# Kernel tuning notes

Measured on AMD Instinct MI355X. Metric: run time of the kernel, lower is better.

## Reference

```python
import jax, jax.numpy as jnp
import numpy as np


def setup_inputs() -> dict:
    key = jax.random.key(0)
    k1, k2, k3 = jax.random.split(key, 3)
    b, c, h, w = 4, 64, 64, 64
    content = jax.random.normal(k1, (b, c, h, w), dtype=jnp.float32)
    content_s = jax.random.normal(k2, (b, c, h, w), dtype=jnp.float32)
    style = jax.random.normal(k3, (b, c, h, w), dtype=jnp.float32)
    return {"content": content, "content_s": content_s, "style": style}


def reference(content, content_s, style):
    b, c, h, w = content.shape
    hw = h * w
    Fc = content.reshape(b, c, hw)      # [b, c, HW]
    Fs = content_s.reshape(b, c, hw)    # [b, c, HW]
    Fst = style.reshape(b, c, hw)       # [b, c, HW]
    # S[b, q, k] = sum_c Fc[b, c, q] * Fs[b, c, k]  (Fc transposed as in torch)
    S = jnp.einsum('bcq,bck->bqk', Fc, Fs)
    S = jax.nn.softmax(S, axis=-1)
    # O = style @ S^T : O[b, c, q] = sum_k Fst[b, c, k] * S[b, q, k]
    O = jnp.einsum('bck,bqk->bcq', Fst, S).reshape(b, c, h, w)
    return jnp.concatenate((content, O), axis=1)
```

## Files before the change

### kernel.cpp

```cpp
#include <hip/hip_runtime.h>
#include <math.h>


#define Bb 4
#define Cc 64
#define HWs 4096
#define RLOG2E 1.44269504088896340736f
#define DEFER_THR 6.0f

typedef _Float16 half8 __attribute__((ext_vector_type(8)));
typedef _Float16 half4 __attribute__((ext_vector_type(4)));
typedef float floatx4 __attribute__((ext_vector_type(4)));
typedef unsigned uint2v __attribute__((ext_vector_type(2)));

__global__ __launch_bounds__(256) void prep_k(const float* __restrict__ content,
                                              const float* __restrict__ Fs,
                                              const float* __restrict__ Fst,
                                              float* __restrict__ out,
                                              _Float16* __restrict__ Kt,
                                              _Float16* __restrict__ Vt) {
    const int bid = blockIdx.x;
    const int t = threadIdx.x;
    if (bid < 1024) {
        int i4 = bid * 256 + t;
        const float4* c4 = (const float4*)content;
        const float4* v4 = (const float4*)Fst;
        float4* o4 = (float4*)out;
        int b = i4 >> 16, rem = i4 & 65535;
        o4[(size_t)b * 131072 + rem] = c4[i4];
        float4 v = v4[i4];
        half4 h;
        h[0] = (_Float16)v.x; h[1] = (_Float16)v.y;
        h[2] = (_Float16)v.z; h[3] = (_Float16)v.w;
        *(half4*)(Vt + (size_t)i4 * 4) = h;
    } else {
        __shared__ _Float16 T[16][72];
        int e = bid - 1024;
        int b = e >> 8;
        int hw0 = (e & 255) * 16;
        const float* sb = Fs + (size_t)b * Cc * HWs;
        {
            int c = t >> 2, x4 = (t & 3) * 4;
            float4 v = *(const float4*)(sb + (size_t)c * HWs + hw0 + x4);
            T[x4 + 0][c] = (_Float16)v.x;
            T[x4 + 1][c] = (_Float16)v.y;
            T[x4 + 2][c] = (_Float16)v.z;
            T[x4 + 3][c] = (_Float16)v.w;
        }
        __syncthreads();
        if (t < 128) {
            int row = t >> 3, g = t & 7;
            _Float16* db = Kt + (size_t)b * HWs * Cc;
            *(half8*)(db + (size_t)(hw0 + row) * Cc + g * 8) = *(half8*)&T[row][g * 8];
        }
    }
}

template <int NS>
__global__ __launch_bounds__(256, 4) void attn_k(const float* __restrict__ Fc,
                                                 const _Float16* __restrict__ Kt,
                                                 const _Float16* __restrict__ Vt,
                                                 _Float16* __restrict__ Opart,
                                                 float2* __restrict__ ml) {
    constexpr int TPS = 64 / NS;
    const int tid  = threadIdx.x;
    const int w    = tid >> 6;
    const int lane = tid & 63;
    const int quad = lane >> 4;
    const int l15  = lane & 15;
    const int qg = blockIdx.x & 31;
    const int b  = (blockIdx.x >> 5) & 3;
    const int s  = blockIdx.x >> 7;
    const int k0base = s * TPS * 64;
    const int qA = qg * 128 + w * 32 + l15;
    const int qB = qA + 16;

    __shared__ _Float16 Kl[2][64 * 64];
    __shared__ _Float16 Vl[2][64 * 64];

    const float*    Fcb = Fc + (size_t)b * Cc * HWs;
    const _Float16* Kb  = Kt + (size_t)b * HWs * Cc;
    const _Float16* Vb  = Vt + (size_t)b * Cc * HWs;

    const bool isK  = tid < 128;
    const int  sl   = tid & 127;
    const int  srow = sl >> 3;
    const int  sjg  = sl & 7;
    const int  ssw  = (sjg ^ (srow & 7)) * 8;

    half8 qf[2][2];
    #pragma unroll
    for (int j = 0; j < 8; ++j) {
        qf[0][0][j] = (_Float16)(Fcb[(size_t)(quad * 8 + j) * HWs + qA] * RLOG2E);
        qf[0][1][j] = (_Float16)(Fcb[(size_t)(32 + quad * 8 + j) * HWs + qA] * RLOG2E);
        qf[1][0][j] = (_Float16)(Fcb[(size_t)(quad * 8 + j) * HWs + qB] * RLOG2E);
        qf[1][1][j] = (_Float16)(Fcb[(size_t)(32 + quad * 8 + j) * HWs + qB] * RLOG2E);
    }

    half8 st[4];
    auto stage_load = [&](int kt) {
        int kk0 = k0base + kt * 64;
        #pragma unroll
        for (int i = 0; i < 4; ++i) {
            int row = srow + 16 * i;
            if (isK) st[i] = *(const half8*)(Kb + (size_t)(kk0 + row) * 64 + sjg * 8);
            else     st[i] = *(const half8*)(Vb + (size_t)row * HWs + kk0 + sjg * 8);
        }
    };
    auto stage_write = [&](int p) {
        #pragma unroll
        for (int i = 0; i < 4; ++i) {
            int row = srow + 16 * i;
            if (isK) *(half8*)&Kl[p][row * 64 + ssw] = st[i];
            else     *(half8*)&Vl[p][row * 64 + ssw] = st[i];
        }
    };

    floatx4 acc[2][4];
    floatx4 accl[2];
    #pragma unroll
    for (int g = 0; g < 2; ++g) {
        accl[g] = (floatx4)(0.0f);
        #pragma unroll
        for (int m = 0; m < 4; ++m) acc[g][m] = (floatx4)(0.0f);
    }
    float m_run[2] = {-INFINITY, -INFINITY};

    half8 vone;
    #pragma unroll
    for (int j = 0; j < 8; ++j) vone[j] = (_Float16)1.0f;

    stage_load(0);
    stage_write(0);
    stage_load(1);
    __syncthreads();

    const int swl = (l15 & 7);
    for (int kt = 0; kt < TPS; ++kt) {
        const int p = kt & 1;
        if (kt + 1 < TPS) stage_write(p ^ 1);
        if (kt + 2 < TPS) stage_load(kt + 2);

        floatx4 sv[2][4];
        #pragma unroll
        for (int m = 0; m < 4; ++m) {
            const half8 ka0 = *(const half8*)&Kl[p][(m * 16 + l15) * 64 + ((quad ^ swl) * 8)];
            const half8 ka1 = *(const half8*)&Kl[p][(m * 16 + l15) * 64 + (((4 + quad) ^ swl) * 8)];
            sv[0][m] = __builtin_amdgcn_mfma_f32_16x16x32_f16(ka0, qf[0][0], (floatx4)(0.0f), 0, 0, 0);
            sv[0][m] = __builtin_amdgcn_mfma_f32_16x16x32_f16(ka1, qf[0][1], sv[0][m], 0, 0, 0);
            sv[1][m] = __builtin_amdgcn_mfma_f32_16x16x32_f16(ka0, qf[1][0], (floatx4)(0.0f), 0, 0, 0);
            sv[1][m] = __builtin_amdgcn_mfma_f32_16x16x32_f16(ka1, qf[1][1], sv[1][m], 0, 0, 0);
        }

        half8 pb[2][2];
        #pragma unroll
        for (int g = 0; g < 2; ++g) {
            float mx = sv[g][0][0];
            #pragma unroll
            for (int m = 0; m < 4; ++m)
                #pragma unroll
                for (int r = 0; r < 4; ++r) mx = fmaxf(mx, sv[g][m][r]);
            {
                unsigned mu = __float_as_uint(mx);
                uint2v t32 = __builtin_amdgcn_permlane32_swap(mu, mu, false, false);
                mx = fmaxf(__uint_as_float(t32[0]), __uint_as_float(t32[1]));
                mu = __float_as_uint(mx);
                uint2v t16 = __builtin_amdgcn_permlane16_swap(mu, mu, false, false);
                mx = fmaxf(__uint_as_float(t16[0]), __uint_as_float(t16[1]));
            }
            if (!__all(mx - m_run[g] <= DEFER_THR)) {
                float m_new = fmaxf(m_run[g], mx);
                float alpha = exp2f(m_run[g] - m_new);
                m_run[g] = m_new;
                #pragma unroll
                for (int m = 0; m < 4; ++m) acc[g][m] *= alpha;
                accl[g] *= alpha;
            }
            const float mb = m_run[g];
            unsigned Ap[4], Bp[4];
            #pragma unroll
            for (int m = 0; m < 4; ++m) {
                float e0 = exp2f(sv[g][m][0] - mb);
                float e1 = exp2f(sv[g][m][1] - mb);
                float e2 = exp2f(sv[g][m][2] - mb);
                float e3 = exp2f(sv[g][m][3] - mb);
                Ap[m] = __builtin_bit_cast(unsigned, __builtin_amdgcn_cvt_pkrtz(e0, e1));
                Bp[m] = __builtin_bit_cast(unsigned, __builtin_amdgcn_cvt_pkrtz(e2, e3));
            }
            unsigned pw[2][4];
            { uint2v a = __builtin_amdgcn_permlane32_swap(Ap[0], Ap[1], false, false);
              uint2v u = __builtin_amdgcn_permlane16_swap(a[0], a[1], false, false);
              pw[0][0] = u[0]; pw[0][2] = u[1]; }
            { uint2v a = __builtin_amdgcn_permlane32_swap(Bp[0], Bp[1], false, false);
              uint2v u = __builtin_amdgcn_permlane16_swap(a[0], a[1], false, false);
              pw[0][1] = u[0]; pw[0][3] = u[1]; }
            { uint2v a = __builtin_amdgcn_permlane32_swap(Ap[2], Ap[3], false, false);
              uint2v u = __builtin_amdgcn_permlane16_swap(a[0], a[1], false, false);
              pw[1][0] = u[0]; pw[1][2] = u[1]; }
            { uint2v a = __builtin_amdgcn_permlane32_swap(Bp[2], Bp[3], false, false);
              uint2v u = __builtin_amdgcn_permlane16_swap(a[0], a[1], false, false);
              pw[1][1] = u[0]; pw[1][3] = u[1]; }
            #pragma unroll
            for (int ks = 0; ks < 2; ++ks) {
                union { unsigned u4[4]; half8 h; } z;
                z.u4[0] = pw[ks][0]; z.u4[1] = pw[ks][1];
                z.u4[2] = pw[ks][2]; z.u4[3] = pw[ks][3];
                pb[g][ks] = z.h;
            }
        }

        #pragma unroll
        for (int m = 0; m < 4; ++m) {
            const half8 va0 = *(const half8*)&Vl[p][(m * 16 + l15) * 64 + ((quad ^ swl) * 8)];
            const half8 va1 = *(const half8*)&Vl[p][(m * 16 + l15) * 64 + (((4 + quad) ^ swl) * 8)];
            acc[0][m] = __builtin_amdgcn_mfma_f32_16x16x32_f16(va0, pb[0][0], acc[0][m], 0, 0, 0);
            acc[0][m] = __builtin_amdgcn_mfma_f32_16x16x32_f16(va1, pb[0][1], acc[0][m], 0, 0, 0);
            acc[1][m] = __builtin_amdgcn_mfma_f32_16x16x32_f16(va0, pb[1][0], acc[1][m], 0, 0, 0);
            acc[1][m] = __builtin_amdgcn_mfma_f32_16x16x32_f16(va1, pb[1][1], acc[1][m], 0, 0, 0);
        }
        accl[0] = __builtin_amdgcn_mfma_f32_16x16x32_f16(vone, pb[0][0], accl[0], 0, 0, 0);
        accl[0] = __builtin_amdgcn_mfma_f32_16x16x32_f16(vone, pb[0][1], accl[0], 0, 0, 0);
        accl[1] = __builtin_amdgcn_mfma_f32_16x16x32_f16(vone, pb[1][0], accl[1], 0, 0, 0);
        accl[1] = __builtin_amdgcn_mfma_f32_16x16x32_f16(vone, pb[1][1], accl[1], 0, 0, 0);

        __syncthreads();
    }

    _Float16* op = Opart + ((size_t)(s * Bb + b) * Cc) * HWs;
    #pragma unroll
    for (int g = 0; g < 2; ++g) {
        int q = (g == 0) ? qA : qB;
        #pragma unroll
        for (int m = 0; m < 4; ++m)
            #pragma unroll
            for (int r = 0; r < 4; ++r) {
                int c = m * 16 + quad * 4 + r;
                op[(size_t)c * HWs + q] = (_Float16)acc[g][m][r];
            }
        if (quad == 0)
            ml[((size_t)b * HWs + q) * NS + s] = make_float2(m_run[g], accl[g][0]);
    }
}

template <int NS>
__global__ __launch_bounds__(256) void combine_k(const _Float16* __restrict__ Opart,
                                                 const float2* __restrict__ ml,
                                                 float* __restrict__ out) {
    int idx = blockIdx.x * 256 + threadIdx.x;
    int q = idx & 4095;
    int c = (idx >> 12) & 63;
    int b = idx >> 18;
    const float2* mlp = ml + ((size_t)b * HWs + q) * NS;
    float2 mls[NS];
    #pragma unroll
    for (int s = 0; s < NS; ++s) mls[s] = mlp[s];
    float M = -INFINITY;
    #pragma unroll
    for (int s = 0; s < NS; ++s) M = fmaxf(M, mls[s].x);
    float l = 0.0f, o = 0.0f;
    #pragma unroll
    for (int s = 0; s < NS; ++s) {
        float wgt = exp2f(mls[s].x - M);
        l += wgt * mls[s].y;
        o += wgt * (float)Opart[(((size_t)s * Bb + b) * Cc + c) * HWs + q];
    }
    out[((size_t)b * 2 * Cc + Cc + c) * HWs + q] = o / l;
}

extern "C" void kernel_launch(void* const* d_in, const int* in_sizes, int n_in,
                              void* d_out, int out_size, void* d_ws, size_t ws_size,
                              hipStream_t stream) {
    const float* content   = (const float*)d_in[0];
    const float* content_s = (const float*)d_in[1];
    const float* style     = (const float*)d_in[2];
    float* out = (float*)d_out;

    _Float16* Kt = (_Float16*)d_ws;
    _Float16* Vt = Kt + (size_t)Bb * HWs * Cc;
    _Float16* Opart = Vt + (size_t)Bb * Cc * HWs;

    const size_t base = (size_t)2 * Bb * HWs * Cc * sizeof(_Float16);
    const size_t need8 = base + (size_t)8 * Bb * Cc * HWs * sizeof(_Float16)
                              + (size_t)Bb * HWs * 8 * sizeof(float2);
    const int ns = (ws_size >= need8) ? 8 : 4;
    float2* ml = (float2*)(Opart + (size_t)ns * Bb * Cc * HWs);

    prep_k<<<dim3(2048), dim3(256), 0, stream>>>(content, content_s, style, out, Kt, Vt);
    if (ns == 8) {
        attn_k<8><<<dim3(8 * Bb * 32), dim3(256), 0, stream>>>(content, Kt, Vt, Opart, ml);
        combine_k<8><<<dim3(4096), dim3(256), 0, stream>>>(Opart, ml, out);
    } else {
        attn_k<4><<<dim3(4 * Bb * 32), dim3(256), 0, stream>>>(content, Kt, Vt, Opart, ml);
        combine_k<4><<<dim3(4096), dim3(256), 0, stream>>>(Opart, ml, out);
    }
}
```

Measured before the change: 112.7 us.

## Stage K/V tiles via direct global-to-LDS loads, sum softmax rows in VALU

Replaces the register-staged K/V tile copy (global load into registers, then LDS write) with the global_load_lds builtin, so all four waves asynchronously fill the next LDS buffer one tile ahead. The row-sum is now accumulated with scalar float adds plus a final shuffle reduction instead of extra MFMA against a ones vector, and s_setprio raises wave priority around the MFMA sections. This is meant to free registers and issue slots and to cut MFMA work, at the cost of a shallower prefetch. The row sum now uses the fp32 exponentials rather than the fp16-rounded values used in the PV product.

```diff
diff --git a/kernel.cpp b/kernel.cpp
--- a/kernel.cpp
+++ b/kernel.cpp
@@ -82,11 +82,26 @@
     const _Float16* Kb  = Kt + (size_t)b * HWs * Cc;
     const _Float16* Vb  = Vt + (size_t)b * Cc * HWs;
 
-    const bool isK  = tid < 128;
-    const int  sl   = tid & 127;
-    const int  srow = sl >> 3;
-    const int  sjg  = sl & 7;
-    const int  ssw  = (sjg ^ (srow & 7)) * 8;
+    const int lrow = lane >> 3;
+    const int lj   = lane & 7;
+    const int lsw8 = (lj ^ lrow) * 8;
+    const int r0   = w * 16;
+
+    auto stage = [&](int kt, int p) {
+        const int kk0 = k0base + kt * 64;
+        #pragma unroll
+        for (int c = 0; c < 2; ++c) {
+            const int r = r0 + c * 8 + lrow;
+            __builtin_amdgcn_global_load_lds(
+                (const __attribute__((address_space(1))) void*)(Kb + (size_t)(kk0 + r) * 64 + lsw8),
+                (__attribute__((address_space(3))) void*)&Kl[p][(r0 + c * 8) * 64],
+                16, 0, 0);
+            __builtin_amdgcn_global_load_lds(
+                (const __attribute__((address_space(1))) void*)(Vb + (size_t)r * HWs + kk0 + lsw8),
+                (__attribute__((address_space(3))) void*)&Vl[p][(r0 + c * 8) * 64],
+                16, 0, 0);
+        }
+    };
 
     half8 qf[2][2];
     #pragma unroll
@@ -97,51 +112,24 @@
         qf[1][1][j] = (_Float16)(Fcb[(size_t)(32 + quad * 8 + j) * HWs + qB] * RLOG2E);
     }
 
-    half8 st[4];
-    auto stage_load = [&](int kt) {
-        int kk0 = k0base + kt * 64;
-        #pragma unroll
-        for (int i = 0; i < 4; ++i) {
-            int row = srow + 16 * i;
-            if (isK) st[i] = *(const half8*)(Kb + (size_t)(kk0 + row) * 64 + sjg * 8);
-            else     st[i] = *(const half8*)(Vb + (size_t)row * HWs + kk0 + sjg * 8);
-        }
-    };
-    auto stage_write = [&](int p) {
-        #pragma unroll
-        for (int i = 0; i < 4; ++i) {
-            int row = srow + 16 * i;
-            if (isK) *(half8*)&Kl[p][row * 64 + ssw] = st[i];
-            else     *(half8*)&Vl[p][row * 64 + ssw] = st[i];
-        }
-    };
-
     floatx4 acc[2][4];
-    floatx4 accl[2];
-    #pragma unroll
-    for (int g = 0; g < 2; ++g) {
-        accl[g] = (floatx4)(0.0f);
+    #pragma unroll
+    for (int g = 0; g < 2; ++g)
         #pragma unroll
         for (int m = 0; m < 4; ++m) acc[g][m] = (floatx4)(0.0f);
-    }
     float m_run[2] = {-INFINITY, -INFINITY};
-
-    half8 vone;
-    #pragma unroll
-    for (int j = 0; j < 8; ++j) vone[j] = (_Float16)1.0f;
-
-    stage_load(0);
-    stage_write(0);
-    stage_load(1);
+    float lsum[2] = {0.0f, 0.0f};
+
+    stage(0, 0);
     __syncthreads();
 
     const int swl = (l15 & 7);
     for (int kt = 0; kt < TPS; ++kt) {
         const int p = kt & 1;
-        if (kt + 1 < TPS) stage_write(p ^ 1);
-        if (kt + 2 < TPS) stage_load(kt + 2);
+        if (kt + 1 < TPS) stage(kt + 1, p ^ 1);
 
         floatx4 sv[2][4];
+        __builtin_amdgcn_s_setprio(1);
         #pragma unroll
         for (int m = 0; m < 4; ++m) {
             const half8 ka0 = *(const half8*)&Kl[p][(m * 16 + l15) * 64 + ((quad ^ swl) * 8)];
@@ -151,6 +139,7 @@
             sv[1][m] = __builtin_amdgcn_mfma_f32_16x16x32_f16(ka0, qf[1][0], (floatx4)(0.0f), 0, 0, 0);
             sv[1][m] = __builtin_amdgcn_mfma_f32_16x16x32_f16(ka1, qf[1][1], sv[1][m], 0, 0, 0);
         }
+        __builtin_amdgcn_s_setprio(0);
 
         half8 pb[2][2];
         #pragma unroll
@@ -174,7 +163,7 @@
                 m_run[g] = m_new;
                 #pragma unroll
                 for (int m = 0; m < 4; ++m) acc[g][m] *= alpha;
-                accl[g] *= alpha;
+                lsum[g] *= alpha;
             }
             const float mb = m_run[g];
             unsigned Ap[4], Bp[4];
@@ -184,6 +173,7 @@
                 float e1 = exp2f(sv[g][m][1] - mb);
                 float e2 = exp2f(sv[g][m][2] - mb);
                 float e3 = exp2f(sv[g][m][3] - mb);
+                lsum[g] += (e0 + e1) + (e2 + e3);
                 Ap[m] = __builtin_bit_cast(unsigned, __builtin_amdgcn_cvt_pkrtz(e0, e1));
                 Bp[m] = __builtin_bit_cast(unsigned, __builtin_amdgcn_cvt_pkrtz(e2, e3));
             }
@@ -209,6 +199,7 @@
             }
         }
 
+        __builtin_amdgcn_s_setprio(1);
         #pragma unroll
         for (int m = 0; m < 4; ++m) {
             const half8 va0 = *(const half8*)&Vl[p][(m * 16 + l15) * 64 + ((quad ^ swl) * 8)];
@@ -218,10 +209,7 @@
             acc[1][m] = __builtin_amdgcn_mfma_f32_16x16x32_f16(va0, pb[1][0], acc[1][m], 0, 0, 0);
             acc[1][m] = __builtin_amdgcn_mfma_f32_16x16x32_f16(va1, pb[1][1], acc[1][m], 0, 0, 0);
         }
-        accl[0] = __builtin_amdgcn_mfma_f32_16x16x32_f16(vone, pb[0][0], accl[0], 0, 0, 0);
-        accl[0] = __builtin_amdgcn_mfma_f32_16x16x32_f16(vone, pb[0][1], accl[0], 0, 0, 0);
-        accl[1] = __builtin_amdgcn_mfma_f32_16x16x32_f16(vone, pb[1][0], accl[1], 0, 0, 0);
-        accl[1] = __builtin_amdgcn_mfma_f32_16x16x32_f16(vone, pb[1][1], accl[1], 0, 0, 0);
+        __builtin_amdgcn_s_setprio(0);
 
         __syncthreads();
     }
@@ -229,6 +217,8 @@
     _Float16* op = Opart + ((size_t)(s * Bb + b) * Cc) * HWs;
     #pragma unroll
     for (int g = 0; g < 2; ++g) {
+        lsum[g] += __shfl_xor(lsum[g], 16);
+        lsum[g] += __shfl_xor(lsum[g], 32);
         int q = (g == 0) ? qA : qB;
         #pragma unroll
         for (int m = 0; m < 4; ++m)
@@ -238,7 +228,7 @@
                 op[(size_t)c * HWs + q] = (_Float16)acc[g][m][r];
             }
         if (quad == 0)
-            ml[((size_t)b * HWs + q) * NS + s] = make_float2(m_run[g], accl[g][0]);
+            ml[((size_t)b * HWs + q) * NS + s] = make_float2(m_run[g], lsum[g]);
     }
 }
 
```

Result: no change. 111.2 us (-1.3%).

## Fold running max into MFMA init, fix four splits, use native exp2

Applied to the files above, without the earlier changes.

The attention kernel now starts the QK MFMA accumulators at -m_run, so scores come out already shifted and the per-element subtraction before exp goes away. The threshold check now runs on the per-lane max before the cross-lane reduction, which skips the permlane work when no rescale is needed. The split count is fixed at 4 rather than chosen at runtime (8 when workspace allows), launch bounds drop to 2 waves, V fragments are loaded before the softmax, and exp2f is replaced by the hardware exp2 intrinsic. The cost is a smaller grid of 512 blocks with twice the serial work per block, plus slightly lower exp precision; m_run starting at 0 instead of -inf changes the max-tracking semantics.

```diff
diff --git a/kernel.cpp b/kernel.cpp
--- a/kernel.cpp
+++ b/kernel.cpp
@@ -5,6 +5,8 @@
 #define Bb 4
 #define Cc 64
 #define HWs 4096
+#define SPLITS 4
+#define TILES_PER_SPLIT 16
 #define RLOG2E 1.44269504088896340736f
 #define DEFER_THR 6.0f
 
@@ -12,6 +14,13 @@
 typedef _Float16 half4 __attribute__((ext_vector_type(4)));
 typedef float floatx4 __attribute__((ext_vector_type(4)));
 typedef unsigned uint2v __attribute__((ext_vector_type(2)));
+
+extern "C" __device__ float __ocml_native_exp2_f32(float);
+#if defined(__has_builtin) && __has_builtin(__builtin_amdgcn_exp2f)
+#define EXP2(x) __builtin_amdgcn_exp2f(x)
+#else
+#define EXP2(x) __ocml_native_exp2_f32(x)
+#endif
 
 __global__ __launch_bounds__(256) void prep_k(const float* __restrict__ content,
                                               const float* __restrict__ Fs,
@@ -56,22 +65,20 @@
     }
 }
 
-template <int NS>
-__global__ __launch_bounds__(256, 4) void attn_k(const float* __restrict__ Fc,
+__global__ __launch_bounds__(256, 2) void attn_k(const float* __restrict__ Fc,
                                                  const _Float16* __restrict__ Kt,
                                                  const _Float16* __restrict__ Vt,
                                                  _Float16* __restrict__ Opart,
                                                  float2* __restrict__ ml) {
-    constexpr int TPS = 64 / NS;
     const int tid  = threadIdx.x;
-    const int w    = tid >> 6;
     const int lane = tid & 63;
     const int quad = lane >> 4;
     const int l15  = lane & 15;
+    const int w    = tid >> 6;
     const int qg = blockIdx.x & 31;
     const int b  = (blockIdx.x >> 5) & 3;
     const int s  = blockIdx.x >> 7;
-    const int k0base = s * TPS * 64;
+    const int k0base = s * TILES_PER_SPLIT * 64;
     const int qA = qg * 128 + w * 32 + l15;
     const int qB = qA + 16;
 
@@ -124,7 +131,7 @@
         #pragma unroll
         for (int m = 0; m < 4; ++m) acc[g][m] = (floatx4)(0.0f);
     }
-    float m_run[2] = {-INFINITY, -INFINITY};
+    float m_run[2] = {0.0f, 0.0f};
 
     half8 vone;
     #pragma unroll
@@ -136,54 +143,66 @@
     __syncthreads();
 
     const int swl = (l15 & 7);
-    for (int kt = 0; kt < TPS; ++kt) {
+    for (int kt = 0; kt < TILES_PER_SPLIT; ++kt) {
         const int p = kt & 1;
-        if (kt + 1 < TPS) stage_write(p ^ 1);
-        if (kt + 2 < TPS) stage_load(kt + 2);
+        if (kt + 1 < TILES_PER_SPLIT) stage_write(p ^ 1);
+        if (kt + 2 < TILES_PER_SPLIT) stage_load(kt + 2);
 
         floatx4 sv[2][4];
-        #pragma unroll
-        for (int m = 0; m < 4; ++m) {
-            const half8 ka0 = *(const half8*)&Kl[p][(m * 16 + l15) * 64 + ((quad ^ swl) * 8)];
-            const half8 ka1 = *(const half8*)&Kl[p][(m * 16 + l15) * 64 + (((4 + quad) ^ swl) * 8)];
-            sv[0][m] = __builtin_amdgcn_mfma_f32_16x16x32_f16(ka0, qf[0][0], (floatx4)(0.0f), 0, 0, 0);
-            sv[0][m] = __builtin_amdgcn_mfma_f32_16x16x32_f16(ka1, qf[0][1], sv[0][m], 0, 0, 0);
-            sv[1][m] = __builtin_amdgcn_mfma_f32_16x16x32_f16(ka0, qf[1][0], (floatx4)(0.0f), 0, 0, 0);
-            sv[1][m] = __builtin_amdgcn_mfma_f32_16x16x32_f16(ka1, qf[1][1], sv[1][m], 0, 0, 0);
-        }
+        {
+            floatx4 c0 = (floatx4)(-m_run[0]);
+            floatx4 c1 = (floatx4)(-m_run[1]);
+            #pragma unroll
+            for (int m = 0; m < 4; ++m) {
+                const half8 ka0 = *(const half8*)&Kl[p][(m * 16 + l15) * 64 + ((quad ^ swl) * 8)];
+                const half8 ka1 = *(const half8*)&Kl[p][(m * 16 + l15) * 64 + (((4 + quad) ^ swl) * 8)];
+                sv[0][m] = __builtin_amdgcn_mfma_f32_16x16x32_f16(ka0, qf[0][0], c0, 0, 0, 0);
+                sv[0][m] = __builtin_amdgcn_mfma_f32_16x16x32_f16(ka1, qf[0][1], sv[0][m], 0, 0, 0);
+                sv[1][m] = __builtin_amdgcn_mfma_f32_16x16x32_f16(ka0, qf[1][0], c1, 0, 0, 0);
+                sv[1][m] = __builtin_amdgcn_mfma_f32_16x16x32_f16(ka1, qf[1][1], sv[1][m], 0, 0, 0);
+            }
+        }
+
+        half8 va[4][2];
+        #pragma unroll
+        for (int m = 0; m < 4; ++m)
+            #pragma unroll
+            for (int ks = 0; ks < 2; ++ks)
+                va[m][ks] = *(const half8*)&Vl[p][(m * 16 + l15) * 64 + (((ks * 4 + quad) ^ swl) * 8)];
 
         half8 pb[2][2];
         #pragma unroll
         for (int g = 0; g < 2; ++g) {
-            float mx = sv[g][0][0];
-            #pragma unroll
-            for (int m = 0; m < 4; ++m)
-                #pragma unroll
-                for (int r = 0; r < 4; ++r) mx = fmaxf(mx, sv[g][m][r]);
-            {
+            float mm0 = fmaxf(fmaxf(fmaxf(sv[g][0][0], sv[g][0][1]), sv[g][0][2]), sv[g][0][3]);
+            float mm1 = fmaxf(fmaxf(fmaxf(sv[g][1][0], sv[g][1][1]), sv[g][1][2]), sv[g][1][3]);
+            float mm2 = fmaxf(fmaxf(fmaxf(sv[g][2][0], sv[g][2][1]), sv[g][2][2]), sv[g][2][3]);
+            float mm3 = fmaxf(fmaxf(fmaxf(sv[g][3][0], sv[g][3][1]), sv[g][3][2]), sv[g][3][3]);
+            float mx = fmaxf(fmaxf(fmaxf(mm0, mm1), mm2), mm3);
+            if (!__all(mx <= DEFER_THR)) {
                 unsigned mu = __float_as_uint(mx);
                 uint2v t32 = __builtin_amdgcn_permlane32_swap(mu, mu, false, false);
-                mx = fmaxf(__uint_as_float(t32[0]), __uint_as_float(t32[1]));
-                mu = __float_as_uint(mx);
+                float wmx = fmaxf(__uint_as_float(t32[0]), __uint_as_float(t32[1]));
+                mu = __float_as_uint(wmx);
                 uint2v t16 = __builtin_amdgcn_permlane16_swap(mu, mu, false, false);
-                mx = fmaxf(__uint_as_float(t16[0]), __uint_as_float(t16[1]));
-            }
-            if (!__all(mx - m_run[g] <= DEFER_THR)) {
-                float m_new = fmaxf(m_run[g], mx);
-                float alpha = exp2f(m_run[g] - m_new);
-                m_run[g] = m_new;
+                wmx = fmaxf(__uint_as_float(t16[0]), __uint_as_float(t16[1]));
+                float delta = fmaxf(wmx, 0.0f);
+                float alpha = EXP2(-delta);
+                m_run[g] += delta;
                 #pragma unroll
                 for (int m = 0; m < 4; ++m) acc[g][m] *= alpha;
                 accl[g] *= alpha;
-            }
-            const float mb = m_run[g];
+                #pragma unroll
+                for (int m = 0; m < 4; ++m)
+                    #pragma unroll
+                    for (int r = 0; r < 4; ++r) sv[g][m][r] -= delta;
+            }
             unsigned Ap[4], Bp[4];
             #pragma unroll
             for (int m = 0; m < 4; ++m) {
-                float e0 = exp2f(sv[g][m][0] - mb);
-                float e1 = exp2f(sv[g][m][1] - mb);
-                float e2 = exp2f(sv[g][m][2] - mb);
-                float e3 = exp2f(sv[g][m][3] - mb);
+                float e0 = EXP2(sv[g][m][0]);
+                float e1 = EXP2(sv[g][m][1]);
+                float e2 = EXP2(sv[g][m][2]);
+                float e3 = EXP2(sv[g][m][3]);
                 Ap[m] = __builtin_bit_cast(unsigned, __builtin_amdgcn_cvt_pkrtz(e0, e1));
                 Bp[m] = __builtin_bit_cast(unsigned, __builtin_amdgcn_cvt_pkrtz(e2, e3));
             }
@@ -210,14 +229,12 @@
         }
 
         #pragma unroll
-        for (int m = 0; m < 4; ++m) {
-            const half8 va0 = *(const half8*)&Vl[p][(m * 16 + l15) * 64 + ((quad ^ swl) * 8)];
-            const half8 va1 = *(const half8*)&Vl[p][(m * 16 + l15) * 64 + (((4 + quad) ^ swl) * 8)];
-            acc[0][m] = __builtin_amdgcn_mfma_f32_16x16x32_f16(va0, pb[0][0], acc[0][m], 0, 0, 0);
-            acc[0][m] = __builtin_amdgcn_mfma_f32_16x16x32_f16(va1, pb[0][1], acc[0][m], 0, 0, 0);
-            acc[1][m] = __builtin_amdgcn_mfma_f32_16x16x32_f16(va0, pb[1][0], acc[1][m], 0, 0, 0);
-            acc[1][m] = __builtin_amdgcn_mfma_f32_16x16x32_f16(va1, pb[1][1], acc[1][m], 0, 0, 0);
-        }
+        for (int m = 0; m < 4; ++m)
+            #pragma unroll
+            for (int g = 0; g < 2; ++g) {
+                acc[g][m] = __builtin_amdgcn_mfma_f32_16x16x32_f16(va[m][0], pb[g][0], acc[g][m], 0, 0, 0);
+                acc[g][m] = __builtin_amdgcn_mfma_f32_16x16x32_f16(va[m][1], pb[g][1], acc[g][m], 0, 0, 0);
+            }
         accl[0] = __builtin_amdgcn_mfma_f32_16x16x32_f16(vone, pb[0][0], accl[0], 0, 0, 0);
         accl[0] = __builtin_amdgcn_mfma_f32_16x16x32_f16(vone, pb[0][1], accl[0], 0, 0, 0);
         accl[1] = __builtin_amdgcn_mfma_f32_16x16x32_f16(vone, pb[1][0], accl[1], 0, 0, 0);
@@ -226,7 +243,7 @@
         __syncthreads();
     }
 
-    _Float16* op = Opart + ((size_t)(s * Bb + b) * Cc) * HWs;
+    _Float16* op = Opart + (((size_t)s * Bb + b) * Cc) * HWs;
     #pragma unroll
     for (int g = 0; g < 2; ++g) {
         int q = (g == 0) ? qA : qB;
@@ -238,11 +255,10 @@
                 op[(size_t)c * HWs + q] = (_Float16)acc[g][m][r];
             }
         if (quad == 0)
-            ml[((size_t)b * HWs + q) * NS + s] = make_float2(m_run[g], accl[g][0]);
+            ml[((size_t)b * HWs + q) * SPLITS + s] = make_float2(m_run[g], accl[g][0]);
     }
 }
 
-template <int NS>
 __global__ __launch_bounds__(256) void combine_k(const _Float16* __restrict__ Opart,
                                                  const float2* __restrict__ ml,
                                                  float* __restrict__ out) {
@@ -250,17 +266,17 @@
     int q = idx & 4095;
     int c = (idx >> 12) & 63;
     int b = idx >> 18;
-    const float2* mlp = ml + ((size_t)b * HWs + q) * NS;
-    float2 mls[NS];
-    #pragma unroll
-    for (int s = 0; s < NS; ++s) mls[s] = mlp[s];
+    const float2* mlp = ml + ((size_t)b * HWs + q) * SPLITS;
+    float2 mls[SPLITS];
+    #pragma unroll
+    for (int s = 0; s < SPLITS; ++s) mls[s] = mlp[s];
     float M = -INFINITY;
     #pragma unroll
-    for (int s = 0; s < NS; ++s) M = fmaxf(M, mls[s].x);
+    for (int s = 0; s < SPLITS; ++s) M = fmaxf(M, mls[s].x);
     float l = 0.0f, o = 0.0f;
     #pragma unroll
-    for (int s = 0; s < NS; ++s) {
-        float wgt = exp2f(mls[s].x - M);
+    for (int s = 0; s < SPLITS; ++s) {
+        float wgt = EXP2(mls[s].x - M);
         l += wgt * mls[s].y;
         o += wgt * (float)Opart[(((size_t)s * Bb + b) * Cc + c) * HWs + q];
     }
@@ -278,19 +294,9 @@
     _Float16* Kt = (_Float16*)d_ws;
     _Float16* Vt = Kt + (size_t)Bb * HWs * Cc;
     _Float16* Opart = Vt + (size_t)Bb * Cc * HWs;
-
-    const size_t base = (size_t)2 * Bb * HWs * Cc * sizeof(_Float16);
-    const size_t need8 = base + (size_t)8 * Bb * Cc * HWs * sizeof(_Float16)
-                              + (size_t)Bb * HWs * 8 * sizeof(float2);
-    const int ns = (ws_size >= need8) ? 8 : 4;
-    float2* ml = (float2*)(Opart + (size_t)ns * Bb * Cc * HWs);
+    float2*   ml = (float2*)(Opart + (size_t)SPLITS * Bb * Cc * HWs);
 
     prep_k<<<dim3(2048), dim3(256), 0, stream>>>(content, content_s, style, out, Kt, Vt);
-    if (ns == 8) {
-        attn_k<8><<<dim3(8 * Bb * 32), dim3(256), 0, stream>>>(content, Kt, Vt, Opart, ml);
-        combine_k<8><<<dim3(4096), dim3(256), 0, stream>>>(Opart, ml, out);
-    } else {
-        attn_k<4><<<dim3(4 * Bb * 32), dim3(256), 0, stream>>>(content, Kt, Vt, Opart, ml);
-        combine_k<4><<<dim3(4096), dim3(256), 0, stream>>>(Opart, ml, out);
-    }
+    attn_k<<<dim3(SPLITS * Bb * 32), dim3(256), 0, stream>>>(content, Kt, Vt, Opart, ml);
+    combine_k<<<dim3(4096), dim3(256), 0, stream>>>(Opart, ml, out);
 }
```

Result: faster. 100.2 us, median of 3 (-11.1%).
